# Performance work log

Measured on AMD Instinct MI355X. Metric: run time of the kernel, lower is better.

Reference implementation:

```python
import jax, jax.numpy as jnp
import numpy as np

B, N, F_IN = 8, 1024, 64
HEADS = 8
D = F_IN  # out_features per head (in_features == out_features)


def setup_inputs() -> dict:
    key = jax.random.key(0)
    ks = jax.random.split(key, 5)
    stdv = 1.0 / np.sqrt(F_IN * HEADS)
    h = jax.random.normal(ks[0], (B, N, F_IN), dtype=jnp.float32)
    adj = jnp.ones((B, N, N), dtype=jnp.float32)  # passed but unused by the module
    W = jax.random.uniform(ks[1], (F_IN, D * HEADS), minval=-stdv, maxval=stdv, dtype=jnp.float32)
    a = jax.random.uniform(ks[2], (2 * D, 1), minval=-stdv, maxval=stdv, dtype=jnp.float32)
    out_W = jax.random.normal(ks[3], (D * HEADS, F_IN), dtype=jnp.float32) / np.sqrt(D * HEADS)
    out_b = jnp.zeros((F_IN,), dtype=jnp.float32)
    return {"h": h, "adj": adj, "W": W, "a": a, "out_W": out_W, "out_b": out_b}


def reference(h, adj, W, a, out_W, out_b):
    Bv, Nv, _ = h.shape
    Dh = W.shape[1] // HEADS
    # Wh: [B, N, H, D]
    Wh = (h @ W).reshape(Bv, Nv, HEADS, Dh)
    # Additive attention decomposed: e[b,i,j,h] = leaky_relu(Wh[b,i,h].a_src + Wh[b,j,h].a_dst)
    a_src = jnp.einsum('bnhd,d->bnh', Wh, a[:Dh, 0])
    a_dst = jnp.einsum('bnhd,d->bnh', Wh, a[Dh:, 0])
    e = jax.nn.leaky_relu(a_src[:, :, None, :] + a_dst[:, None, :, :], negative_slope=0.01)  # [B,N,N,H]
    # Module applies softmax over dim=1 (the first node axis i)
    attn = jax.nn.softmax(e, axis=1)  # [B,N,N,H]
    # h_prime[b,i,h,:] = sum_j attn[b,i,j,h] * Wh[b,j,h,:]
    h_prime = jnp.einsum('bijh,bjhd->bihd', attn, Wh).reshape(Bv, Nv, HEADS * Dh)
    return h_prime @ out_W + out_b
```

## Files before the change

kernel.cpp:

```cpp
#include <hip/hip_runtime.h>


#define B_  8
#define N_  1024
#define H_  8
#define D_  64
#define BH_ 64

__global__ __launch_bounds__(256) void k_wh(
    const float* __restrict__ h, const float* __restrict__ W,
    const float* __restrict__ a,
    float* __restrict__ Wh, float* __restrict__ sArr, float* __restrict__ tArr) {
  __shared__ float hL[16 * 64];
  __shared__ float whL[16 * 512];
  __shared__ float aL[128];
  const int tid = threadIdx.x;
  const int row0 = blockIdx.x * 16;
  const int b = row0 >> 10;
  for (int i = tid; i < 16 * 64; i += 256) hL[i] = h[row0 * 64 + i];
  if (tid < 128) aL[tid] = a[tid];
  __syncthreads();

  float acc0[16], acc1[16];
#pragma unroll
  for (int r = 0; r < 16; ++r) { acc0[r] = 0.f; acc1[r] = 0.f; }
  for (int k = 0; k < 64; ++k) {
    const float w0 = W[k * 512 + tid];
    const float w1 = W[k * 512 + tid + 256];
#pragma unroll
    for (int r = 0; r < 16; ++r) {
      const float hv = hL[r * 64 + k];
      acc0[r] += hv * w0;
      acc1[r] += hv * w1;
    }
  }
  const int hh0 = tid >> 6, d0 = tid & 63;
  const int hh1 = (tid + 256) >> 6;
#pragma unroll
  for (int r = 0; r < 16; ++r) {
    const int n = (row0 + r) & (N_ - 1);
    whL[r * 512 + tid] = acc0[r];
    whL[r * 512 + tid + 256] = acc1[r];
    Wh[((b * H_ + hh0) * N_ + n) * D_ + d0] = acc0[r];
    Wh[((b * H_ + hh1) * N_ + n) * D_ + d0] = acc1[r];
  }
  __syncthreads();
  if (tid < 128) {
    const int r = tid >> 3, hh = tid & 7;
    const int n = (row0 + r) & (N_ - 1);
    float accS = 0.f, accT = 0.f;
    for (int jj = 0; jj < 64; ++jj) {
      const int d = (jj + tid) & 63;
      const float wv = whL[r * 512 + hh * 64 + d];
      accS += wv * aL[d];
      accT += wv * aL[64 + d];
    }
    sArr[(b * H_ + hh) * N_ + n] = accS;
    tArr[(b * H_ + hh) * N_ + n] = accT;
  }
}

__global__ __launch_bounds__(1024) void k_sort(
    const float* __restrict__ sArr, const float* __restrict__ tArr,
    const float* __restrict__ Wh,
    float* __restrict__ tsv, int* __restrict__ tsi,
    float* __restrict__ uArr, float* __restrict__ vArr,
    float* __restrict__ cOff1, float* __restrict__ cOff2) {
  __shared__ float tv[1024];
  __shared__ int   ti[1024];
  __shared__ float sv[1024];
  __shared__ float cum1[1024], cum001[1024];
  __shared__ float uL[1024], vL[1024];
  __shared__ float cs1[16 * 64], cs2[16 * 64];
  const int tid = threadIdx.x;
  const int bh = blockIdx.x;
  tv[tid] = tArr[bh * N_ + tid];
  ti[tid] = tid;
  sv[tid] = sArr[bh * N_ + tid];
  __syncthreads();

  for (int size = 2; size <= 1024; size <<= 1) {
    for (int stride = size >> 1; stride > 0; stride >>= 1) {
      const int i = tid, j = i ^ stride;
      if (j > i) {
        const bool up = ((i & size) == 0);
        float av = tv[i], bv = tv[j];
        if ((av > bv) == up) {
          tv[i] = bv; tv[j] = av;
          int t_ = ti[i]; ti[i] = ti[j]; ti[j] = t_;
        }
        float as = sv[i], bs = sv[j];
        if ((as > bs) == up) { sv[i] = bs; sv[j] = as; }
      }
      __syncthreads();
    }
  }

  cum1[tid] = expf(sv[tid]);
  cum001[tid] = expf(0.01f * sv[tid]);
  __syncthreads();
  for (int off = 1; off < 1024; off <<= 1) {
    float x1 = 0.f, x2 = 0.f;
    if (tid >= off) { x1 = cum1[tid - off]; x2 = cum001[tid - off]; }
    __syncthreads();
    cum1[tid] += x1; cum001[tid] += x2;
    __syncthreads();
  }
  const float totalHi = cum1[1023];

  {
    const float tj = tv[tid];
    const float th = -tj;
    int lo = 0, hi = 1024;
    while (lo < hi) { const int mid = (lo + hi) >> 1; if (sv[mid] <= th) lo = mid + 1; else hi = mid; }
    const float S_lo = (lo > 0) ? cum001[lo - 1] : 0.f;
    const float S_hi = totalHi - ((lo > 0) ? cum1[lo - 1] : 0.f);
    const float et = expf(tj), et001 = expf(0.01f * tj);
    const float Z = et * S_hi + et001 * S_lo;
    const float u = et / Z, v = et001 / Z;
    uArr[bh * N_ + tid] = u; vArr[bh * N_ + tid] = v;
    tsv[bh * N_ + tid] = tj; tsi[bh * N_ + tid] = ti[tid];
    uL[tid] = u; vL[tid] = v;
  }
  __syncthreads();

  const int c = tid >> 6, d = tid & 63;
  float s1 = 0.f, s2 = 0.f;
  for (int jj = 0; jj < 64; ++jj) {
    const int k = c * 64 + jj;
    const int j = ti[k];
    const float w = Wh[(bh * N_ + j) * D_ + d];
    s1 += uL[k] * w;
    s2 += vL[k] * w;
  }
  cs1[c * 64 + d] = s1; cs2[c * 64 + d] = s2;
  __syncthreads();
  float o1 = 0.f, o2 = 0.f;
  for (int cc = 0; cc < 16; ++cc) {
    if (cc < c) { o1 += cs1[cc * 64 + d]; o2 += cs2[cc * 64 + d]; }
  }
  cOff1[(bh * 16 + c) * 64 + d] = o1;
  cOff2[(bh * 16 + c) * 64 + d] = o2;
}

__global__ __launch_bounds__(64) void k_inc(
    const float* __restrict__ Wh, const int* __restrict__ tsi,
    const float* __restrict__ uArr, const float* __restrict__ vArr,
    const float* __restrict__ cOff1, const float* __restrict__ cOff2,
    float* __restrict__ INC1, float* __restrict__ INC2) {
  const int blk = blockIdx.x;
  const int bh = blk >> 4, c = blk & 15;
  const int d = threadIdx.x;
  float r1 = cOff1[blk * 64 + d];
  float r2 = cOff2[blk * 64 + d];
  const int base = bh * N_;
#pragma unroll 4
  for (int jj = 0; jj < 64; ++jj) {
    const int k = c * 64 + jj;
    const int j = tsi[base + k];
    const float u = uArr[base + k], v = vArr[base + k];
    const float w = Wh[(base + j) * D_ + d];
    r1 += u * w;
    r2 += v * w;
    INC1[(base + k) * D_ + d] = r1;
    INC2[(base + k) * D_ + d] = r2;
  }
}

__global__ __launch_bounds__(512) void k_out(
    const float* __restrict__ sArr, const float* __restrict__ tsv,
    const float* __restrict__ INC1, const float* __restrict__ INC2,
    const float* __restrict__ outW, const float* __restrict__ outb,
    float* __restrict__ out) {
  __shared__ float hpL[16 * 512];
  __shared__ float part[8 * 8 * 64];
  __shared__ int   rkI[16 * 8];
  __shared__ float esL[16 * 8], es001L[16 * 8];
  const int tid = threadIdx.x;
  const int row0 = blockIdx.x * 16;
  const int b = row0 >> 10;

  if (tid < 128) {
    const int r = tid >> 3, hh = tid & 7;
    const int bh = b * H_ + hh;
    const int n = (row0 + r) & (N_ - 1);
    const float si = sArr[bh * N_ + n];
    const float th = -si;
    const float* tvp = tsv + bh * N_;
    int lo = 0, hi = 1024;
    while (lo < hi) { const int mid = (lo + hi) >> 1; if (tvp[mid] <= th) lo = mid + 1; else hi = mid; }
    rkI[tid] = lo;
    esL[tid] = expf(si);
    es001L[tid] = expf(0.01f * si);
  }
  __syncthreads();

  {
    const int hh = tid >> 6, d = tid & 63;
    const int bh = b * H_ + hh;
    const float T1 = INC1[(bh * N_ + (N_ - 1)) * D_ + d];
    for (int r = 0; r < 16; ++r) {
      const int rk = rkI[r * 8 + hh];
      float i1 = 0.f, i2 = 0.f;
      if (rk > 0) {
        i1 = INC1[(bh * N_ + rk - 1) * D_ + d];
        i2 = INC2[(bh * N_ + rk - 1) * D_ + d];
      }
      hpL[r * 512 + hh * 64 + d] =
          esL[r * 8 + hh] * (T1 - i1) + es001L[r * 8 + hh] * i2;
    }
  }
  __syncthreads();

  const int cc = tid & 63, p = tid >> 6;
  float acc[16];
#pragma unroll
  for (int r = 0; r < 16; ++r) acc[r] = 0.f;
  for (int k = p * 64; k < p * 64 + 64; ++k) {
    const float wv = outW[k * 64 + cc];
#pragma unroll
    for (int r = 0; r < 16; ++r) acc[r] += hpL[r * 512 + k] * wv;
  }
  for (int half = 0; half < 2; ++half) {
#pragma unroll
    for (int r = 0; r < 8; ++r) part[(p * 8 + r) * 64 + cc] = acc[half * 8 + r];
    __syncthreads();
    {
      const int r = tid >> 6, c2 = tid & 63;
      float ssum = 0.f;
#pragma unroll
      for (int p2 = 0; p2 < 8; ++p2) ssum += part[(p2 * 8 + r) * 64 + c2];
      out[(row0 + half * 8 + r) * 64 + c2] = outb[c2] + ssum;
    }
    __syncthreads();
  }
}

extern "C" void kernel_launch(void* const* d_in, const int* in_sizes, int n_in,
                              void* d_out, int out_size, void* d_ws, size_t ws_size,
                              hipStream_t stream) {
  const float* h    = (const float*)d_in[0];
  const float* W    = (const float*)d_in[2];
  const float* a    = (const float*)d_in[3];
  const float* outW = (const float*)d_in[4];
  const float* outb = (const float*)d_in[5];
  float* out = (float*)d_out;

  float* ws   = (float*)d_ws;
  float* Wh   = ws;
  float* sArr = Wh + (size_t)BH_ * N_ * D_;
  float* tArr = sArr + BH_ * N_;
  float* tsv  = tArr + BH_ * N_;
  int*   tsi  = (int*)(tsv + BH_ * N_);
  float* uArr = (float*)(tsi + BH_ * N_);
  float* vArr = uArr + BH_ * N_;
  float* cOff1 = vArr + BH_ * N_;
  float* cOff2 = cOff1 + BH_ * 16 * 64;
  float* INC1 = cOff2 + BH_ * 16 * 64;
  float* INC2 = INC1 + (size_t)BH_ * N_ * D_;

  hipLaunchKernelGGL(k_wh,   dim3((B_ * N_) / 16), dim3(256), 0, stream,
                     h, W, a, Wh, sArr, tArr);
  hipLaunchKernelGGL(k_sort, dim3(BH_), dim3(1024), 0, stream,
                     sArr, tArr, Wh, tsv, tsi, uArr, vArr, cOff1, cOff2);
  hipLaunchKernelGGL(k_inc,  dim3(BH_ * 16), dim3(64), 0, stream,
                     Wh, tsi, uArr, vArr, cOff1, cOff2, INC1, INC2);
  hipLaunchKernelGGL(k_out,  dim3((B_ * N_) / 16), dim3(512), 0, stream,
                     sArr, tsv, INC1, INC2, outW, outb, out);
}
```

Before: 167.4 us.

## Register-resident bitonic sort with wave shuffles, move rank search into sort kernel, finer chunks

```diff
diff --git a/kernel.cpp b/kernel.cpp
--- a/kernel.cpp
+++ b/kernel.cpp
@@ -6,6 +6,8 @@
 #define H_  8
 #define D_  64
 #define BH_ 64
+#define CH_ 32
+#define CL_ 32
 
 __global__ __launch_bounds__(256) void k_wh(
     const float* __restrict__ h, const float* __restrict__ W,
@@ -63,84 +65,118 @@
 __global__ __launch_bounds__(1024) void k_sort(
     const float* __restrict__ sArr, const float* __restrict__ tArr,
     const float* __restrict__ Wh,
-    float* __restrict__ tsv, int* __restrict__ tsi,
-    float* __restrict__ uArr, float* __restrict__ vArr,
+    int* __restrict__ tsi, float* __restrict__ uArr, float* __restrict__ vArr,
+    int* __restrict__ qrk,
     float* __restrict__ cOff1, float* __restrict__ cOff2) {
-  __shared__ float tv[1024];
-  __shared__ int   ti[1024];
-  __shared__ float sv[1024];
-  __shared__ float cum1[1024], cum001[1024];
+  __shared__ float sL[1024];
+  __shared__ float tvL[1024];
+  __shared__ int   tiL[1024];
+  __shared__ float cum1L[1024], cum001L[1024];
   __shared__ float uL[1024], vL[1024];
-  __shared__ float cs1[16 * 64], cs2[16 * 64];
+  __shared__ float cs1[CH_ * 64], cs2[CH_ * 64];
+  __shared__ float ws1[16], ws2[16];
   const int tid = threadIdx.x;
+  const int lane = tid & 63;
+  const int wv_ = tid >> 6;
   const int bh = blockIdx.x;
-  tv[tid] = tArr[bh * N_ + tid];
-  ti[tid] = tid;
-  sv[tid] = sArr[bh * N_ + tid];
-  __syncthreads();
+
+  const float orig_s = sArr[bh * N_ + tid];
+  float sv_r = orig_s;
+  float tv_r = tArr[bh * N_ + tid];
+  int   ti_r = tid;
 
   for (int size = 2; size <= 1024; size <<= 1) {
     for (int stride = size >> 1; stride > 0; stride >>= 1) {
-      const int i = tid, j = i ^ stride;
-      if (j > i) {
-        const bool up = ((i & size) == 0);
-        float av = tv[i], bv = tv[j];
-        if ((av > bv) == up) {
-          tv[i] = bv; tv[j] = av;
-          int t_ = ti[i]; ti[i] = ti[j]; ti[j] = t_;
-        }
-        float as = sv[i], bs = sv[j];
-        if ((as > bs) == up) { sv[i] = bs; sv[j] = as; }
+      const bool up = ((tid & size) == 0);
+      const bool lower = ((tid & stride) == 0);
+      float psv, ptv; int pti;
+      if (stride >= 64) {
+        sL[tid] = sv_r; tvL[tid] = tv_r; tiL[tid] = ti_r;
+        __syncthreads();
+        const int p = tid ^ stride;
+        psv = sL[p]; ptv = tvL[p]; pti = tiL[p];
+        __syncthreads();
+      } else {
+        psv = __shfl_xor(sv_r, stride);
+        ptv = __shfl_xor(tv_r, stride);
+        pti = __shfl_xor(ti_r, stride);
       }
-      __syncthreads();
-    }
-  }
-
-  cum1[tid] = expf(sv[tid]);
-  cum001[tid] = expf(0.01f * sv[tid]);
-  __syncthreads();
-  for (int off = 1; off < 1024; off <<= 1) {
-    float x1 = 0.f, x2 = 0.f;
-    if (tid >= off) { x1 = cum1[tid - off]; x2 = cum001[tid - off]; }
+      const bool sameDir = (up == lower);
+      const bool pLessS = (psv < sv_r);
+      if (pLessS == sameDir) sv_r = psv;
+      const bool pLessT = (ptv < tv_r) || (ptv == tv_r && pti < ti_r);
+      if (pLessT == sameDir) { tv_r = ptv; ti_r = pti; }
+    }
+  }
+  sL[tid] = sv_r; tvL[tid] = tv_r; tiL[tid] = ti_r;
+
+  float c1 = __expf(sv_r) , c001 = __expf(0.01f * sv_r);
+  {
+    float a1 = c1, a2 = c001;
+#pragma unroll
+    for (int off = 1; off < 64; off <<= 1) {
+      const float x1 = __shfl_up(a1, off);
+      const float x2 = __shfl_up(a2, off);
+      if (lane >= off) { a1 += x1; a2 += x2; }
+    }
+    if (lane == 63) { ws1[wv_] = a1; ws2[wv_] = a2; }
     __syncthreads();
-    cum1[tid] += x1; cum001[tid] += x2;
-    __syncthreads();
-  }
-  const float totalHi = cum1[1023];
+    float o1 = 0.f, o2 = 0.f;
+    for (int ww = 0; ww < 16; ++ww) {
+      if (ww < wv_) { o1 += ws1[ww]; o2 += ws2[ww]; }
+    }
+    c1 = a1 + o1; c001 = a2 + o2;
+  }
+  cum1L[tid] = c1; cum001L[tid] = c001;
+  __syncthreads();
+  const float totalHi = cum1L[1023];
 
   {
-    const float tj = tv[tid];
+    const float tj = tv_r;
     const float th = -tj;
     int lo = 0, hi = 1024;
-    while (lo < hi) { const int mid = (lo + hi) >> 1; if (sv[mid] <= th) lo = mid + 1; else hi = mid; }
-    const float S_lo = (lo > 0) ? cum001[lo - 1] : 0.f;
-    const float S_hi = totalHi - ((lo > 0) ? cum1[lo - 1] : 0.f);
-    const float et = expf(tj), et001 = expf(0.01f * tj);
+    while (lo < hi) { const int mid = (lo + hi) >> 1; if (sL[mid] <= th) lo = mid + 1; else hi = mid; }
+    const float S_lo = (lo > 0) ? cum001L[lo - 1] : 0.f;
+    const float S_hi = totalHi - ((lo > 0) ? cum1L[lo - 1] : 0.f);
+    const float et = __expf(tj), et001 = __expf(0.01f * tj);
     const float Z = et * S_hi + et001 * S_lo;
     const float u = et / Z, v = et001 / Z;
+    uL[tid] = u; vL[tid] = v;
     uArr[bh * N_ + tid] = u; vArr[bh * N_ + tid] = v;
-    tsv[bh * N_ + tid] = tj; tsi[bh * N_ + tid] = ti[tid];
-    uL[tid] = u; vL[tid] = v;
+    tsi[bh * N_ + tid] = ti_r;
+  }
+
+  {
+    const float th = -orig_s;
+    int lo = 0, hi = 1024;
+    while (lo < hi) { const int mid = (lo + hi) >> 1; if (tvL[mid] <= th) lo = mid + 1; else hi = mid; }
+    qrk[bh * N_ + tid] = lo;
   }
   __syncthreads();
 
   const int c = tid >> 6, d = tid & 63;
-  float s1 = 0.f, s2 = 0.f;
-  for (int jj = 0; jj < 64; ++jj) {
-    const int k = c * 64 + jj;
-    const int j = ti[k];
-    const float w = Wh[(bh * N_ + j) * D_ + d];
-    s1 += uL[k] * w;
-    s2 += vL[k] * w;
-  }
-  cs1[c * 64 + d] = s1; cs2[c * 64 + d] = s2;
-  __syncthreads();
-  float o1 = 0.f, o2 = 0.f;
-  for (int cc = 0; cc < 16; ++cc) {
-    if (cc < c) { o1 += cs1[cc * 64 + d]; o2 += cs2[cc * 64 + d]; }
-  }
-  cOff1[(bh * 16 + c) * 64 + d] = o1;
-  cOff2[(bh * 16 + c) * 64 + d] = o2;
+#pragma unroll
+  for (int half = 0; half < 2; ++half) {
+    const int cc = c + half * 16;
+    float s1 = 0.f, s2 = 0.f;
+    for (int k2 = 0; k2 < CL_; ++k2) {
+      const int k = cc * CL_ + k2;
+      const int j = tiL[k];
+      const float w = Wh[(bh * N_ + j) * D_ + d];
+      s1 += uL[k] * w;
+      s2 += vL[k] * w;
+    }
+    cs1[cc * 64 + d] = s1; cs2[cc * 64 + d] = s2;
+  }
+  __syncthreads();
+#pragma unroll
+  for (int half = 0; half < 2; ++half) {
+    const int cc = c + half * 16;
+    float o1 = 0.f, o2 = 0.f;
+    for (int m = 0; m < cc; ++m) { o1 += cs1[m * 64 + d]; o2 += cs2[m * 64 + d]; }
+    cOff1[(bh * CH_ + cc) * 64 + d] = o1;
+    cOff2[(bh * CH_ + cc) * 64 + d] = o2;
+  }
 }
 
 __global__ __launch_bounds__(64) void k_inc(
@@ -149,14 +185,14 @@
     const float* __restrict__ cOff1, const float* __restrict__ cOff2,
     float* __restrict__ INC1, float* __restrict__ INC2) {
   const int blk = blockIdx.x;
-  const int bh = blk >> 4, c = blk & 15;
+  const int bh = blk >> 5, c = blk & (CH_ - 1);
   const int d = threadIdx.x;
   float r1 = cOff1[blk * 64 + d];
   float r2 = cOff2[blk * 64 + d];
   const int base = bh * N_;
-#pragma unroll 4
-  for (int jj = 0; jj < 64; ++jj) {
-    const int k = c * 64 + jj;
+#pragma unroll 8
+  for (int k2 = 0; k2 < CL_; ++k2) {
+    const int k = c * CL_ + k2;
     const int j = tsi[base + k];
     const float u = uArr[base + k], v = vArr[base + k];
     const float w = Wh[(base + j) * D_ + d];
@@ -168,7 +204,7 @@
 }
 
 __global__ __launch_bounds__(512) void k_out(
-    const float* __restrict__ sArr, const float* __restrict__ tsv,
+    const float* __restrict__ sArr, const int* __restrict__ qrk,
     const float* __restrict__ INC1, const float* __restrict__ INC2,
     const float* __restrict__ outW, const float* __restrict__ outb,
     float* __restrict__ out) {
@@ -185,13 +221,9 @@
     const int bh = b * H_ + hh;
     const int n = (row0 + r) & (N_ - 1);
     const float si = sArr[bh * N_ + n];
-    const float th = -si;
-    const float* tvp = tsv + bh * N_;
-    int lo = 0, hi = 1024;
-    while (lo < hi) { const int mid = (lo + hi) >> 1; if (tvp[mid] <= th) lo = mid + 1; else hi = mid; }
-    rkI[tid] = lo;
-    esL[tid] = expf(si);
-    es001L[tid] = expf(0.01f * si);
+    rkI[tid] = qrk[bh * N_ + n];
+    esL[tid] = __expf(si);
+    es001L[tid] = __expf(0.01f * si);
   }
   __syncthreads();
 
@@ -217,9 +249,9 @@
 #pragma unroll
   for (int r = 0; r < 16; ++r) acc[r] = 0.f;
   for (int k = p * 64; k < p * 64 + 64; ++k) {
-    const float wv = outW[k * 64 + cc];
-#pragma unroll
-    for (int r = 0; r < 16; ++r) acc[r] += hpL[r * 512 + k] * wv;
+    const float wvv = outW[k * 64 + cc];
+#pragma unroll
+    for (int r = 0; r < 16; ++r) acc[r] += hpL[r * 512 + k] * wvv;
   }
   for (int half = 0; half < 2; ++half) {
 #pragma unroll
@@ -250,21 +282,21 @@
   float* Wh   = ws;
   float* sArr = Wh + (size_t)BH_ * N_ * D_;
   float* tArr = sArr + BH_ * N_;
-  float* tsv  = tArr + BH_ * N_;
-  int*   tsi  = (int*)(tsv + BH_ * N_);
+  int*   tsi  = (int*)(tArr + BH_ * N_);
   float* uArr = (float*)(tsi + BH_ * N_);
   float* vArr = uArr + BH_ * N_;
-  float* cOff1 = vArr + BH_ * N_;
-  float* cOff2 = cOff1 + BH_ * 16 * 64;
-  float* INC1 = cOff2 + BH_ * 16 * 64;
+  int*   qrk  = (int*)(vArr + BH_ * N_);
+  float* cOff1 = (float*)(qrk + BH_ * N_);
+  float* cOff2 = cOff1 + BH_ * CH_ * 64;
+  float* INC1 = cOff2 + BH_ * CH_ * 64;
   float* INC2 = INC1 + (size_t)BH_ * N_ * D_;
 
   hipLaunchKernelGGL(k_wh,   dim3((B_ * N_) / 16), dim3(256), 0, stream,
                      h, W, a, Wh, sArr, tArr);
   hipLaunchKernelGGL(k_sort, dim3(BH_), dim3(1024), 0, stream,
-                     sArr, tArr, Wh, tsv, tsi, uArr, vArr, cOff1, cOff2);
-  hipLaunchKernelGGL(k_inc,  dim3(BH_ * 16), dim3(64), 0, stream,
+                     sArr, tArr, Wh, tsi, uArr, vArr, qrk, cOff1, cOff2);
+  hipLaunchKernelGGL(k_inc,  dim3(BH_ * CH_), dim3(64), 0, stream,
                      Wh, tsi, uArr, vArr, cOff1, cOff2, INC1, INC2);
   hipLaunchKernelGGL(k_out,  dim3((B_ * N_) / 16), dim3(512), 0, stream,
-                     sArr, tsv, INC1, INC2, outW, outb, out);
-}
+                     sArr, qrk, INC1, INC2, outW, outb, out);
+}
```

Result: faster. 155.4 us (-7.1%).
